# Performance work log

Measured on AMD Instinct MI355X. Metric: run time of the kernel, lower is better.

The kernel has to match this reference:

```python
import jax, jax.numpy as jnp
import numpy as np

N_EMBED = 1024
EMBED_DIM = 256

def setup_inputs() -> dict:
    key = jax.random.key(0)
    k1, k2 = jax.random.split(key)
    hidden_states = jax.random.normal(k1, (64, 32, 32, EMBED_DIM), dtype=jnp.float32)
    emb_weights = jax.random.normal(k2, (N_EMBED, EMBED_DIM), dtype=jnp.float32)
    return {"hidden_states": hidden_states, "emb_weights": emb_weights}

def reference(hidden_states, emb_weights):
    # flatten (B,H,W,C) -> (N, C) with C == embed_dim
    z_flat = hidden_states.reshape((-1, EMBED_DIM))
    # squared distance: ||z||^2 + ||e||^2 - 2 z.e
    distance = (
        jnp.sum(z_flat ** 2, axis=1, keepdims=True)
        + jnp.sum(emb_weights ** 2, axis=1)
        - 2.0 * jnp.dot(z_flat, emb_weights.T)
    )  # (N, n_embed)
    min_encoding_indices = jnp.argmin(distance, axis=1)  # (N,)
    z_q = jnp.take(emb_weights, min_encoding_indices, axis=0).reshape(hidden_states.shape)
    min_encoding_indices = min_encoding_indices.reshape(hidden_states.shape[0], -1)
    return z_q, min_encoding_indices
```

## Files before the change

kernel.cpp:

```cpp
#include <hip/hip_runtime.h>

typedef _Float16 half8  __attribute__((ext_vector_type(8)));
typedef _Float16 half4  __attribute__((ext_vector_type(4)));
typedef float    float4v __attribute__((ext_vector_type(4)));
typedef float    float8v __attribute__((ext_vector_type(8)));

#define N_ROWS  65536
#define N_CODES 1024
#define DIM     256
#define BM      64
#define NBLKS   (N_ROWS / BM)

__global__ __launch_bounds__(64)
void vq_prep(const float* __restrict__ emb, float* __restrict__ e_norm,
             _Float16* __restrict__ e_frag, int* __restrict__ count) {
    const int c = blockIdx.x, lane = threadIdx.x;
    const int l15 = c & 15, nt = c >> 4;
    if (count && c == 0 && lane == 0) *count = 0;
    float4v v = ((const float4v*)(emb + (size_t)c * DIM))[lane];
    half4 h, l;
    float ss = 0.f;
    #pragma unroll
    for (int j = 0; j < 4; ++j) {
        float x = v[j];
        ss += x * x;
        _Float16 hh = (_Float16)x;
        h[j] = hh;
        l[j] = (_Float16)(x - (float)hh);
    }
    const int ks = lane >> 3, q = (lane >> 1) & 3, jb = (lane & 1) * 4;
    _Float16* p = e_frag + ((size_t)(nt * 8 + ks)) * 1024 + (q * 16 + l15) * 8 + jb;
    *(half4*)p = h;
    *(half4*)(p + 512) = l;
    #pragma unroll
    for (int m = 32; m >= 1; m >>= 1) ss += __shfl_xor(ss, m, 64);
    if (lane == 0) e_norm[c] = ss;
}

__global__ __launch_bounds__(256, 2)
void vq_screen(const float* __restrict__ z,
               const _Float16* __restrict__ e_frag,
               const float* __restrict__ e_norm,
               const float* __restrict__ emb,
               float* __restrict__ zq,
               float* __restrict__ idxf,
               int* __restrict__ count,
               int* __restrict__ list) {
    __shared__ _Float16 sA[32 * 512];
    __shared__ float    s_nrm[N_CODES];
    __shared__ float    s_znrm[BM];
    __shared__ float    s_red[4];
    __shared__ float4   s_best[BM][5];
    __shared__ int      s_idx[BM];

    const int t = threadIdx.x;
    const int w = t >> 6, lane = t & 63, quad = lane >> 4, l15 = lane & 15;
    const int rowblk = blockIdx.x * BM;

    float n0 = e_norm[t], n1 = e_norm[t + 256], n2 = e_norm[t + 512], n3 = e_norm[t + 768];
    s_nrm[t] = n0; s_nrm[t + 256] = n1; s_nrm[t + 512] = n2; s_nrm[t + 768] = n3;
    float mx = fmaxf(fmaxf(n0, n1), fmaxf(n2, n3));
    #pragma unroll
    for (int m = 1; m < 64; m <<= 1) mx = fmaxf(mx, __shfl_xor(mx, m, 64));
    if (lane == 0) s_red[w] = mx;

    float ss = 0.f;
    #pragma unroll
    for (int i = 0; i < 8; ++i) {
        const int row = w * 16 + l15;
        const int col = i * 32 + quad * 8;
        float8v v = *(const float8v*)(z + (size_t)(rowblk + row) * DIM + col);
        half8 h;
        #pragma unroll
        for (int j = 0; j < 8; ++j) {
            float x = v[j];
            ss += x * x;
            h[j] = (_Float16)x;
        }
        *(half8*)(sA + (size_t)(w * 8 + i) * 512 + lane * 8) = h;
    }
    ss += __shfl_xor(ss, 16, 64);
    ss += __shfl_xor(ss, 32, 64);
    if (quad == 0) s_znrm[w * 16 + l15] = ss;
    __syncthreads();

    for (int pass = 0; pass < 2; ++pass) {
        const int ntbase = w * 16 + pass * 8;
        float4v acc[4][8] = {};

        #pragma unroll
        for (int ks = 0; ks < 8; ++ks) {
            half8 bh[8];
            #pragma unroll
            for (int nt = 0; nt < 8; ++nt)
                bh[nt] = *(const half8*)(e_frag + ((size_t)((ntbase + nt) * 8 + ks)) * 1024 + lane * 8);
            __builtin_amdgcn_s_setprio(1);
            #pragma unroll
            for (int mt = 0; mt < 4; ++mt) {
                half8 ah = *(const half8*)(sA + (size_t)(mt * 8 + ks) * 512 + lane * 8);
                #pragma unroll
                for (int nt = 0; nt < 8; ++nt)
                    acc[mt][nt] = __builtin_amdgcn_mfma_f32_16x16x32_f16(ah, bh[nt], acc[mt][nt], 0, 0, 0);
            }
            __builtin_amdgcn_s_setprio(0);
        }

        float nrm[8]; int cg[8];
        #pragma unroll
        for (int nt = 0; nt < 8; ++nt) {
            cg[nt]  = (ntbase + nt) * 16 + l15;
            nrm[nt] = s_nrm[cg[nt]];
        }
        #pragma unroll
        for (int mt = 0; mt < 4; ++mt) {
            #pragma unroll
            for (int r = 0; r < 4; ++r) {
                float m1 = nrm[0] - 2.0f * acc[mt][0][r]; int i1 = cg[0];
                float m2 = 1e30f;
                #pragma unroll
                for (int nt = 1; nt < 8; ++nt) {
                    float s = nrm[nt] - 2.0f * acc[mt][nt][r];
                    if (s < m1) { m2 = m1; m1 = s; i1 = cg[nt]; }
                    else m2 = fminf(m2, s);
                }
                #pragma unroll
                for (int m = 1; m < 16; m <<= 1) {
                    float o1 = __shfl_xor(m1, m, 64);
                    int   oi = __shfl_xor(i1, m, 64);
                    float o2 = __shfl_xor(m2, m, 64);
                    if (o1 < m1 || (o1 == m1 && oi < i1)) {
                        m2 = fminf(m1, o2); m1 = o1; i1 = oi;
                    } else {
                        m2 = fminf(m2, o1);
                    }
                }
                if (l15 == 0) {
                    const int row = mt * 16 + quad * 4 + r;
                    if (pass == 0) {
                        float4 pr; pr.x = m1; pr.y = (float)i1; pr.z = m2; pr.w = 0.f;
                        s_best[row][w] = pr;
                    } else {
                        float4 pv = s_best[row][w];
                        float4 pr;
                        if (m1 < pv.x) { pr.x = m1; pr.y = (float)i1; pr.z = fminf(pv.x, m2); }
                        else           { pr.x = pv.x; pr.y = pv.y;     pr.z = fminf(pv.z, m1); }
                        pr.w = 0.f;
                        s_best[row][w] = pr;
                    }
                }
            }
        }
    }
    __syncthreads();

    if (t < BM) {
        float4 b0 = s_best[t][0];
        float m1 = b0.x, fi = b0.y, m2 = b0.z;
        #pragma unroll
        for (int s = 1; s < 4; ++s) {
            float4 bv = s_best[t][s];
            if (bv.x < m1 || (bv.x == m1 && bv.y < fi)) {
                m2 = fminf(m1, bv.z); m1 = bv.x; fi = bv.y;
            } else {
                m2 = fminf(m2, bv.x);
            }
        }
        s_idx[t] = (int)fi;
        idxf[rowblk + t] = fi;
        float emax = sqrtf(fmaxf(fmaxf(s_red[0], s_red[1]), fmaxf(s_red[2], s_red[3])));
        float T = 0.005f * sqrtf(s_znrm[t]) * emax + 0.05f;
        if (m2 - m1 <= T) {
            int pos = atomicAdd(count, 1);
            list[pos] = rowblk + t;
        }
    }
    __syncthreads();

    const float4v* emb4 = (const float4v*)emb;
    float4v* zq4 = (float4v*)zq;
    const int rr = t >> 2, cb = t & 3;
    const int code = s_idx[rr];
    #pragma unroll
    for (int i = 0; i < 16; ++i) {
        const int chunk = cb + i * 4;
        zq4[(size_t)(rowblk + rr) * 64 + chunk] = emb4[(size_t)code * 64 + chunk];
    }
}

__global__ __launch_bounds__(256, 2)
void vq_exact(const float* __restrict__ z,
              const _Float16* __restrict__ e_frag,
              const float* __restrict__ e_norm,
              const float* __restrict__ emb,
              float* __restrict__ zq,
              float* __restrict__ idxf,
              const int* __restrict__ count,
              const int* __restrict__ list) {
    const int cnt = *count;
    const int base = blockIdx.x * BM;
    if (base >= cnt) return;

    __shared__ _Float16 sA[32 * 2 * 512];
    __shared__ float    s_nrm[N_CODES];
    __shared__ float2   s_best[BM][5];
    __shared__ int      s_idx[BM];
    __shared__ int      s_rows[BM];

    const int t = threadIdx.x;
    const int w = t >> 6, lane = t & 63, quad = lane >> 4, l15 = lane & 15;

    if (t < BM) {
        int slot = base + t;
        s_rows[t] = list[slot < cnt ? slot : cnt - 1];
    }
    s_nrm[t]       = e_norm[t];
    s_nrm[t + 256] = e_norm[t + 256];
    s_nrm[t + 512] = e_norm[t + 512];
    s_nrm[t + 768] = e_norm[t + 768];
    __syncthreads();

    #pragma unroll
    for (int i = 0; i < 8; ++i) {
        const int row = w * 16 + l15;
        const int grow = s_rows[row];
        const int col = i * 32 + quad * 8;
        float8v v = *(const float8v*)(z + (size_t)grow * DIM + col);
        half8 h, lo;
        #pragma unroll
        for (int j = 0; j < 8; ++j) {
            float x = v[j];
            _Float16 hh = (_Float16)x;
            h[j] = hh;
            lo[j] = (_Float16)(x - (float)hh);
        }
        _Float16* p = sA + (size_t)((w * 8 + i) * 2) * 512 + lane * 8;
        *(half8*)p = h;
        *(half8*)(p + 512) = lo;
    }
    __syncthreads();

    for (int pass = 0; pass < 2; ++pass) {
        const int ntbase = w * 16 + pass * 8;
        float4v acc[4][8] = {};

        #pragma unroll
        for (int ks = 0; ks < 8; ++ks) {
            half8 bh[8], bl[8];
            #pragma unroll
            for (int nt = 0; nt < 8; ++nt) {
                const _Float16* bp = e_frag + ((size_t)((ntbase + nt) * 8 + ks)) * 1024 + lane * 8;
                bh[nt] = *(const half8*)bp;
                bl[nt] = *(const half8*)(bp + 512);
            }
            __builtin_amdgcn_s_setprio(1);
            #pragma unroll
            for (int mt = 0; mt < 4; ++mt) {
                const _Float16* ap = sA + (size_t)((mt * 8 + ks) * 2) * 512 + lane * 8;
                half8 ah = *(const half8*)ap;
                half8 al = *(const half8*)(ap + 512);
                #pragma unroll
                for (int nt = 0; nt < 8; ++nt)
                    acc[mt][nt] = __builtin_amdgcn_mfma_f32_16x16x32_f16(ah, bh[nt], acc[mt][nt], 0, 0, 0);
                #pragma unroll
                for (int nt = 0; nt < 8; ++nt)
                    acc[mt][nt] = __builtin_amdgcn_mfma_f32_16x16x32_f16(ah, bl[nt], acc[mt][nt], 0, 0, 0);
                #pragma unroll
                for (int nt = 0; nt < 8; ++nt)
                    acc[mt][nt] = __builtin_amdgcn_mfma_f32_16x16x32_f16(al, bh[nt], acc[mt][nt], 0, 0, 0);
            }
            __builtin_amdgcn_s_setprio(0);
        }

        float nrm[8]; int cg[8];
        #pragma unroll
        for (int nt = 0; nt < 8; ++nt) {
            cg[nt]  = (ntbase + nt) * 16 + l15;
            nrm[nt] = s_nrm[cg[nt]];
        }
        #pragma unroll
        for (int mt = 0; mt < 4; ++mt) {
            #pragma unroll
            for (int r = 0; r < 4; ++r) {
                float bs = nrm[0] - 2.0f * acc[mt][0][r]; int bi = cg[0];
                #pragma unroll
                for (int nt = 1; nt < 8; ++nt) {
                    float s = nrm[nt] - 2.0f * acc[mt][nt][r];
                    if (s < bs) { bs = s; bi = cg[nt]; }
                }
                #pragma unroll
                for (int m = 1; m < 16; m <<= 1) {
                    float s2 = __shfl_xor(bs, m, 64);
                    int   i2 = __shfl_xor(bi, m, 64);
                    if (s2 < bs || (s2 == bs && i2 < bi)) { bs = s2; bi = i2; }
                }
                if (l15 == 0) {
                    const int row = mt * 16 + quad * 4 + r;
                    if (pass == 0) {
                        float2 pr; pr.x = bs; pr.y = (float)bi;
                        s_best[row][w] = pr;
                    } else {
                        float2 pv = s_best[row][w];
                        if (bs < pv.x) {
                            float2 pr; pr.x = bs; pr.y = (float)bi;
                            s_best[row][w] = pr;
                        }
                    }
                }
            }
        }
    }
    __syncthreads();

    if (t < BM) {
        float2 p0 = s_best[t][0];
        float bs = p0.x, bi = p0.y;
        #pragma unroll
        for (int s = 1; s < 4; ++s) {
            float2 pv = s_best[t][s];
            if (pv.x < bs || (pv.x == bs && pv.y < bi)) { bs = pv.x; bi = pv.y; }
        }
        s_idx[t] = (int)bi;
        idxf[s_rows[t]] = bi;
    }
    __syncthreads();

    const float4v* emb4 = (const float4v*)emb;
    float4v* zq4 = (float4v*)zq;
    const int rr = t >> 2, cb = t & 3;
    const int grow = s_rows[rr];
    const int code = s_idx[rr];
    #pragma unroll
    for (int i = 0; i < 16; ++i) {
        const int chunk = cb + i * 4;
        zq4[(size_t)grow * 64 + chunk] = emb4[(size_t)code * 64 + chunk];
    }
}

__global__ __launch_bounds__(256, 2)
void vq_main(const float* __restrict__ z,
             const _Float16* __restrict__ e_frag,
             const float* __restrict__ e_norm,
             const float* __restrict__ emb,
             float* __restrict__ zq,
             float* __restrict__ idxf,
             int fused_gather) {
    __shared__ _Float16 sA[32 * 2 * 512];
    __shared__ float    s_nrm[N_CODES];
    __shared__ float2   s_best[BM][5];
    __shared__ int      s_idx[BM];

    const int t = threadIdx.x;
    const int w = t >> 6, lane = t & 63, quad = lane >> 4, l15 = lane & 15;
    const int rowblk = blockIdx.x * BM;

    s_nrm[t]       = e_norm[t];
    s_nrm[t + 256] = e_norm[t + 256];
    s_nrm[t + 512] = e_norm[t + 512];
    s_nrm[t + 768] = e_norm[t + 768];

    #pragma unroll
    for (int i = 0; i < 8; ++i) {
        const int row = w * 16 + l15;
        const int col = i * 32 + quad * 8;
        float8v v = *(const float8v*)(z + (size_t)(rowblk + row) * DIM + col);
        half8 h, lo;
        #pragma unroll
        for (int j = 0; j < 8; ++j) {
            float x = v[j];
            _Float16 hh = (_Float16)x;
            h[j] = hh;
            lo[j] = (_Float16)(x - (float)hh);
        }
        _Float16* p = sA + (size_t)((w * 8 + i) * 2) * 512 + lane * 8;
        *(half8*)p = h;
        *(half8*)(p + 512) = lo;
    }
    __syncthreads();

    for (int pass = 0; pass < 2; ++pass) {
        const int ntbase = w * 16 + pass * 8;
        float4v acc[4][8] = {};

        #pragma unroll
        for (int ks = 0; ks < 8; ++ks) {
            half8 bh[8], bl[8];
            #pragma unroll
            for (int nt = 0; nt < 8; ++nt) {
                const _Float16* bp = e_frag + ((size_t)((ntbase + nt) * 8 + ks)) * 1024 + lane * 8;
                bh[nt] = *(const half8*)bp;
                bl[nt] = *(const half8*)(bp + 512);
            }
            __builtin_amdgcn_s_setprio(1);
            #pragma unroll
            for (int mt = 0; mt < 4; ++mt) {
                const _Float16* ap = sA + (size_t)((mt * 8 + ks) * 2) * 512 + lane * 8;
                half8 ah = *(const half8*)ap;
                half8 al = *(const half8*)(ap + 512);
                #pragma unroll
                for (int nt = 0; nt < 8; ++nt)
                    acc[mt][nt] = __builtin_amdgcn_mfma_f32_16x16x32_f16(ah, bh[nt], acc[mt][nt], 0, 0, 0);
                #pragma unroll
                for (int nt = 0; nt < 8; ++nt)
                    acc[mt][nt] = __builtin_amdgcn_mfma_f32_16x16x32_f16(ah, bl[nt], acc[mt][nt], 0, 0, 0);
                #pragma unroll
                for (int nt = 0; nt < 8; ++nt)
                    acc[mt][nt] = __builtin_amdgcn_mfma_f32_16x16x32_f16(al, bh[nt], acc[mt][nt], 0, 0, 0);
            }
            __builtin_amdgcn_s_setprio(0);
        }

        float nrm[8]; int cg[8];
        #pragma unroll
        for (int nt = 0; nt < 8; ++nt) {
            cg[nt]  = (ntbase + nt) * 16 + l15;
            nrm[nt] = s_nrm[cg[nt]];
        }
        #pragma unroll
        for (int mt = 0; mt < 4; ++mt) {
            #pragma unroll
            for (int r = 0; r < 4; ++r) {
                float bs = nrm[0] - 2.0f * acc[mt][0][r]; int bi = cg[0];
                #pragma unroll
                for (int nt = 1; nt < 8; ++nt) {
                    float s = nrm[nt] - 2.0f * acc[mt][nt][r];
                    if (s < bs) { bs = s; bi = cg[nt]; }
                }
                #pragma unroll
                for (int m = 1; m < 16; m <<= 1) {
                    float s2 = __shfl_xor(bs, m, 64);
                    int   i2 = __shfl_xor(bi, m, 64);
                    if (s2 < bs || (s2 == bs && i2 < bi)) { bs = s2; bi = i2; }
                }
                if (l15 == 0) {
                    const int row = mt * 16 + quad * 4 + r;
                    if (pass == 0) {
                        float2 pr; pr.x = bs; pr.y = (float)bi;
                        s_best[row][w] = pr;
                    } else {
                        float2 pv = s_best[row][w];
                        if (bs < pv.x) {
                            float2 pr; pr.x = bs; pr.y = (float)bi;
                            s_best[row][w] = pr;
                        }
                    }
                }
            }
        }
    }
    __syncthreads();

    if (t < BM) {
        float2 p0 = s_best[t][0];
        float bs = p0.x, bi = p0.y;
        #pragma unroll
        for (int s = 1; s < 4; ++s) {
            float2 pv = s_best[t][s];
            if (pv.x < bs || (pv.x == bs && pv.y < bi)) { bs = pv.x; bi = pv.y; }
        }
        s_idx[t] = (int)bi;
        idxf[rowblk + t] = bi;
    }

    if (!fused_gather) return;
    __syncthreads();

    const float4v* emb4 = (const float4v*)emb;
    float4v* zq4 = (float4v*)zq;
    const int rr = t >> 2, cb = t & 3;
    const int code = s_idx[rr];
    #pragma unroll
    for (int i = 0; i < 16; ++i) {
        const int chunk = cb + i * 4;
        zq4[(size_t)(rowblk + rr) * 64 + chunk] = emb4[(size_t)code * 64 + chunk];
    }
}

__global__ __launch_bounds__(256)
void vq_gather(const float* __restrict__ emb,
               const float* __restrict__ idxf,
               float* __restrict__ zq) {
    const int tid  = blockIdx.x * 256 + threadIdx.x;
    const int r    = tid >> 6;
    const int lane = tid & 63;
    const int idx  = (int)idxf[r];
    const float4* ep = (const float4*)(emb + (size_t)idx * DIM);
    ((float4*)(zq + (size_t)r * DIM))[lane] = ep[lane];
}

extern "C" void kernel_launch(void* const* d_in, const int* in_sizes, int n_in,
                              void* d_out, int out_size, void* d_ws, size_t ws_size,
                              hipStream_t stream) {
    const float* z   = (const float*)d_in[0];
    const float* emb = (const float*)d_in[1];

    float* zq   = (float*)d_out;
    float* idxf = zq + (size_t)N_ROWS * DIM;

    const size_t efrag_sz = (size_t)N_CODES * DIM * 2 * sizeof(_Float16);
    const size_t list_sz  = (size_t)N_ROWS * sizeof(int);
    const size_t need_p   = 4096 + efrag_sz + 4096 + list_sz;

    if (ws_size >= need_p) {
        float*    e_norm = (float*)d_ws;
        _Float16* e_frag = (_Float16*)((char*)d_ws + 4096);
        int*      count  = (int*)((char*)d_ws + 4096 + efrag_sz);
        int*      list   = (int*)((char*)d_ws + 4096 + efrag_sz + 4096);
        vq_prep<<<N_CODES, 64, 0, stream>>>(emb, e_norm, e_frag, count);
        vq_screen<<<NBLKS, 256, 0, stream>>>(z, e_frag, e_norm, emb, zq, idxf, count, list);
        vq_exact<<<NBLKS, 256, 0, stream>>>(z, e_frag, e_norm, emb, zq, idxf, count, list);
    } else {
        const size_t need = 4096 + efrag_sz;
        const int in_ws = (ws_size >= need);
        char* base = in_ws ? (char*)d_ws : (char*)d_out;
        float*    e_norm = (float*)base;
        _Float16* e_frag = (_Float16*)(base + 4096);
        vq_prep<<<N_CODES, 64, 0, stream>>>(emb, e_norm, e_frag, (int*)0);
        vq_main<<<NBLKS, 256, 0, stream>>>(z, e_frag, e_norm, emb, zq, idxf, in_ws);
        if (!in_ws)
            vq_gather<<<(N_ROWS * 64) / 256, 256, 0, stream>>>(emb, idxf, zq);
    }
}
```

Before: 217.5 us.

## Tighten screen error bound and split exact rescoring across code octants

The fp16 screening threshold now comes from the actual low-part residual norms of z and the codebook, rather than a fixed relative factor. This should flag fewer rows for exact rescoring. The exact pass is split into vq_resc, which uses 8 blocks per group of 64 flagged rows, each covering one eighth of the codes and merging results through 64-bit packed atomicMin. A separate vq_fix kernel then writes the indices and the gather. This adds a kernel launch and extra atomics and workspace, in exchange for more parallelism and less rescoring work.

```diff
diff --git a/kernel.cpp b/kernel.cpp
--- a/kernel.cpp
+++ b/kernel.cpp
@@ -11,45 +11,63 @@
 #define BM      64
 #define NBLKS   (N_ROWS / BM)
 
+__device__ __forceinline__ unsigned long long packScore(float s, int code) {
+    unsigned u = __float_as_uint(s);
+    u ^= (u >> 31) ? 0xFFFFFFFFu : 0x80000000u;
+    return ((unsigned long long)u << 32) | (unsigned)code;
+}
+
 __global__ __launch_bounds__(64)
 void vq_prep(const float* __restrict__ emb, float* __restrict__ e_norm,
-             _Float16* __restrict__ e_frag, int* __restrict__ count) {
+             float* __restrict__ el2, _Float16* __restrict__ e_frag,
+             int* __restrict__ count) {
     const int c = blockIdx.x, lane = threadIdx.x;
     const int l15 = c & 15, nt = c >> 4;
     if (count && c == 0 && lane == 0) *count = 0;
     float4v v = ((const float4v*)(emb + (size_t)c * DIM))[lane];
     half4 h, l;
-    float ss = 0.f;
+    float ss = 0.f, ssl = 0.f;
     #pragma unroll
     for (int j = 0; j < 4; ++j) {
         float x = v[j];
         ss += x * x;
         _Float16 hh = (_Float16)x;
+        float xl = x - (float)hh;
+        ssl += xl * xl;
         h[j] = hh;
-        l[j] = (_Float16)(x - (float)hh);
+        l[j] = (_Float16)xl;
     }
     const int ks = lane >> 3, q = (lane >> 1) & 3, jb = (lane & 1) * 4;
     _Float16* p = e_frag + ((size_t)(nt * 8 + ks)) * 1024 + (q * 16 + l15) * 8 + jb;
     *(half4*)p = h;
     *(half4*)(p + 512) = l;
     #pragma unroll
-    for (int m = 32; m >= 1; m >>= 1) ss += __shfl_xor(ss, m, 64);
-    if (lane == 0) e_norm[c] = ss;
+    for (int m = 32; m >= 1; m >>= 1) {
+        ss  += __shfl_xor(ss, m, 64);
+        ssl += __shfl_xor(ssl, m, 64);
+    }
+    if (lane == 0) {
+        e_norm[c] = ss;
+        if (el2) el2[c] = ssl;
+    }
 }
 
 __global__ __launch_bounds__(256, 2)
 void vq_screen(const float* __restrict__ z,
                const _Float16* __restrict__ e_frag,
                const float* __restrict__ e_norm,
+               const float* __restrict__ el2,
                const float* __restrict__ emb,
                float* __restrict__ zq,
                float* __restrict__ idxf,
                int* __restrict__ count,
-               int* __restrict__ list) {
+               int* __restrict__ list,
+               unsigned long long* __restrict__ packed) {
     __shared__ _Float16 sA[32 * 512];
     __shared__ float    s_nrm[N_CODES];
     __shared__ float    s_znrm[BM];
-    __shared__ float    s_red[4];
+    __shared__ float    s_zlnrm[BM];
+    __shared__ float    s_red[4], s_redl[4];
     __shared__ float4   s_best[BM][5];
     __shared__ int      s_idx[BM];
 
@@ -60,11 +78,16 @@
     float n0 = e_norm[t], n1 = e_norm[t + 256], n2 = e_norm[t + 512], n3 = e_norm[t + 768];
     s_nrm[t] = n0; s_nrm[t + 256] = n1; s_nrm[t + 512] = n2; s_nrm[t + 768] = n3;
     float mx = fmaxf(fmaxf(n0, n1), fmaxf(n2, n3));
-    #pragma unroll
-    for (int m = 1; m < 64; m <<= 1) mx = fmaxf(mx, __shfl_xor(mx, m, 64));
-    if (lane == 0) s_red[w] = mx;
-
-    float ss = 0.f;
+    float q0 = el2[t], q1 = el2[t + 256], q2 = el2[t + 512], q3 = el2[t + 768];
+    float mxl = fmaxf(fmaxf(q0, q1), fmaxf(q2, q3));
+    #pragma unroll
+    for (int m = 1; m < 64; m <<= 1) {
+        mx  = fmaxf(mx,  __shfl_xor(mx, m, 64));
+        mxl = fmaxf(mxl, __shfl_xor(mxl, m, 64));
+    }
+    if (lane == 0) { s_red[w] = mx; s_redl[w] = mxl; }
+
+    float ss = 0.f, ssl = 0.f;
     #pragma unroll
     for (int i = 0; i < 8; ++i) {
         const int row = w * 16 + l15;
@@ -75,13 +98,18 @@
         for (int j = 0; j < 8; ++j) {
             float x = v[j];
             ss += x * x;
-            h[j] = (_Float16)x;
+            _Float16 hh = (_Float16)x;
+            float xl = x - (float)hh;
+            ssl += xl * xl;
+            h[j] = hh;
         }
         *(half8*)(sA + (size_t)(w * 8 + i) * 512 + lane * 8) = h;
     }
-    ss += __shfl_xor(ss, 16, 64);
-    ss += __shfl_xor(ss, 32, 64);
-    if (quad == 0) s_znrm[w * 16 + l15] = ss;
+    ss  += __shfl_xor(ss, 16, 64);
+    ss  += __shfl_xor(ss, 32, 64);
+    ssl += __shfl_xor(ssl, 16, 64);
+    ssl += __shfl_xor(ssl, 32, 64);
+    if (quad == 0) { s_znrm[w * 16 + l15] = ss; s_zlnrm[w * 16 + l15] = ssl; }
     __syncthreads();
 
     for (int pass = 0; pass < 2; ++pass) {
@@ -167,11 +195,13 @@
         }
         s_idx[t] = (int)fi;
         idxf[rowblk + t] = fi;
-        float emax = sqrtf(fmaxf(fmaxf(s_red[0], s_red[1]), fmaxf(s_red[2], s_red[3])));
-        float T = 0.005f * sqrtf(s_znrm[t]) * emax + 0.05f;
+        float emax  = sqrtf(fmaxf(fmaxf(s_red[0],  s_red[1]),  fmaxf(s_red[2],  s_red[3])));
+        float elmax = sqrtf(fmaxf(fmaxf(s_redl[0], s_redl[1]), fmaxf(s_redl[2], s_redl[3])));
+        float T = 2.0f * (sqrtf(s_zlnrm[t]) * emax + 1.001f * sqrtf(s_znrm[t]) * elmax) + 0.02f;
         if (m2 - m1 <= T) {
             int pos = atomicAdd(count, 1);
             list[pos] = rowblk + t;
+            packed[rowblk + t] = 0xFFFFFFFFFFFFFFFFull;
         }
     }
     __syncthreads();
@@ -188,35 +218,27 @@
 }
 
 __global__ __launch_bounds__(256, 2)
-void vq_exact(const float* __restrict__ z,
-              const _Float16* __restrict__ e_frag,
-              const float* __restrict__ e_norm,
-              const float* __restrict__ emb,
-              float* __restrict__ zq,
-              float* __restrict__ idxf,
-              const int* __restrict__ count,
-              const int* __restrict__ list) {
+void vq_resc(const float* __restrict__ z,
+             const _Float16* __restrict__ e_frag,
+             const float* __restrict__ e_norm,
+             const int* __restrict__ count,
+             const int* __restrict__ list,
+             unsigned long long* __restrict__ packed) {
     const int cnt = *count;
-    const int base = blockIdx.x * BM;
-    if (base >= cnt) return;
+    const int g = blockIdx.x >> 3, oct = blockIdx.x & 7;
+    if (g * BM >= cnt) return;
 
     __shared__ _Float16 sA[32 * 2 * 512];
-    __shared__ float    s_nrm[N_CODES];
     __shared__ float2   s_best[BM][5];
-    __shared__ int      s_idx[BM];
     __shared__ int      s_rows[BM];
 
     const int t = threadIdx.x;
     const int w = t >> 6, lane = t & 63, quad = lane >> 4, l15 = lane & 15;
 
     if (t < BM) {
-        int slot = base + t;
+        int slot = g * BM + t;
         s_rows[t] = list[slot < cnt ? slot : cnt - 1];
     }
-    s_nrm[t]       = e_norm[t];
-    s_nrm[t + 256] = e_norm[t + 256];
-    s_nrm[t + 512] = e_norm[t + 512];
-    s_nrm[t + 768] = e_norm[t + 768];
     __syncthreads();
 
     #pragma unroll
@@ -225,6 +247,152 @@
         const int grow = s_rows[row];
         const int col = i * 32 + quad * 8;
         float8v v = *(const float8v*)(z + (size_t)grow * DIM + col);
+        half8 h, lo;
+        #pragma unroll
+        for (int j = 0; j < 8; ++j) {
+            float x = v[j];
+            _Float16 hh = (_Float16)x;
+            h[j] = hh;
+            lo[j] = (_Float16)(x - (float)hh);
+        }
+        _Float16* p = sA + (size_t)((w * 8 + i) * 2) * 512 + lane * 8;
+        *(half8*)p = h;
+        *(half8*)(p + 512) = lo;
+    }
+    __syncthreads();
+
+    const int ntbase = oct * 8 + w * 2;
+    float4v acc[4][2] = {};
+
+    #pragma unroll
+    for (int ks = 0; ks < 8; ++ks) {
+        half8 bh[2], bl[2];
+        #pragma unroll
+        for (int nt = 0; nt < 2; ++nt) {
+            const _Float16* bp = e_frag + ((size_t)((ntbase + nt) * 8 + ks)) * 1024 + lane * 8;
+            bh[nt] = *(const half8*)bp;
+            bl[nt] = *(const half8*)(bp + 512);
+        }
+        __builtin_amdgcn_s_setprio(1);
+        #pragma unroll
+        for (int mt = 0; mt < 4; ++mt) {
+            const _Float16* ap = sA + (size_t)((mt * 8 + ks) * 2) * 512 + lane * 8;
+            half8 ah = *(const half8*)ap;
+            half8 al = *(const half8*)(ap + 512);
+            #pragma unroll
+            for (int nt = 0; nt < 2; ++nt)
+                acc[mt][nt] = __builtin_amdgcn_mfma_f32_16x16x32_f16(ah, bh[nt], acc[mt][nt], 0, 0, 0);
+            #pragma unroll
+            for (int nt = 0; nt < 2; ++nt)
+                acc[mt][nt] = __builtin_amdgcn_mfma_f32_16x16x32_f16(ah, bl[nt], acc[mt][nt], 0, 0, 0);
+            #pragma unroll
+            for (int nt = 0; nt < 2; ++nt)
+                acc[mt][nt] = __builtin_amdgcn_mfma_f32_16x16x32_f16(al, bh[nt], acc[mt][nt], 0, 0, 0);
+        }
+        __builtin_amdgcn_s_setprio(0);
+    }
+
+    float nrm[2]; int cg[2];
+    #pragma unroll
+    for (int nt = 0; nt < 2; ++nt) {
+        cg[nt]  = (ntbase + nt) * 16 + l15;
+        nrm[nt] = e_norm[cg[nt]];
+    }
+    #pragma unroll
+    for (int mt = 0; mt < 4; ++mt) {
+        #pragma unroll
+        for (int r = 0; r < 4; ++r) {
+            float bs = nrm[0] - 2.0f * acc[mt][0][r]; int bi = cg[0];
+            float s1 = nrm[1] - 2.0f * acc[mt][1][r];
+            if (s1 < bs) { bs = s1; bi = cg[1]; }
+            #pragma unroll
+            for (int m = 1; m < 16; m <<= 1) {
+                float s2 = __shfl_xor(bs, m, 64);
+                int   i2 = __shfl_xor(bi, m, 64);
+                if (s2 < bs || (s2 == bs && i2 < bi)) { bs = s2; bi = i2; }
+            }
+            if (l15 == 0) {
+                float2 pr; pr.x = bs; pr.y = (float)bi;
+                s_best[mt * 16 + quad * 4 + r][w] = pr;
+            }
+        }
+    }
+    __syncthreads();
+
+    if (t < BM) {
+        float2 p0 = s_best[t][0];
+        float bs = p0.x, bi = p0.y;
+        #pragma unroll
+        for (int s = 1; s < 4; ++s) {
+            float2 pv = s_best[t][s];
+            if (pv.x < bs || (pv.x == bs && pv.y < bi)) { bs = pv.x; bi = pv.y; }
+        }
+        atomicMin(&packed[s_rows[t]], packScore(bs, (int)bi));
+    }
+}
+
+__global__ __launch_bounds__(256)
+void vq_fix(const float* __restrict__ emb,
+            const int* __restrict__ count,
+            const int* __restrict__ list,
+            const unsigned long long* __restrict__ packed,
+            float* __restrict__ zq,
+            float* __restrict__ idxf) {
+    const int cnt = *count;
+    const int base = blockIdx.x * BM;
+    if (base >= cnt) return;
+
+    __shared__ int s_rows[BM], s_code[BM];
+    const int t = threadIdx.x;
+    if (t < BM) {
+        int slot = base + t;
+        int row = list[slot < cnt ? slot : cnt - 1];
+        s_rows[t] = row;
+        int code = (int)(unsigned)packed[row];
+        s_code[t] = code;
+        idxf[row] = (float)code;
+    }
+    __syncthreads();
+
+    const float4v* emb4 = (const float4v*)emb;
+    float4v* zq4 = (float4v*)zq;
+    const int rr = t >> 2, cb = t & 3;
+    const int grow = s_rows[rr];
+    const int code = s_code[rr];
+    #pragma unroll
+    for (int i = 0; i < 16; ++i) {
+        const int chunk = cb + i * 4;
+        zq4[(size_t)grow * 64 + chunk] = emb4[(size_t)code * 64 + chunk];
+    }
+}
+
+__global__ __launch_bounds__(256, 2)
+void vq_main(const float* __restrict__ z,
+             const _Float16* __restrict__ e_frag,
+             const float* __restrict__ e_norm,
+             const float* __restrict__ emb,
+             float* __restrict__ zq,
+             float* __restrict__ idxf,
+             int fused_gather) {
+    __shared__ _Float16 sA[32 * 2 * 512];
+    __shared__ float    s_nrm[N_CODES];
+    __shared__ float2   s_best[BM][5];
+    __shared__ int      s_idx[BM];
+
+    const int t = threadIdx.x;
+    const int w = t >> 6, lane = t & 63, quad = lane >> 4, l15 = lane & 15;
+    const int rowblk = blockIdx.x * BM;
+
+    s_nrm[t]       = e_norm[t];
+    s_nrm[t + 256] = e_norm[t + 256];
+    s_nrm[t + 512] = e_norm[t + 512];
+    s_nrm[t + 768] = e_norm[t + 768];
+
+    #pragma unroll
+    for (int i = 0; i < 8; ++i) {
+        const int row = w * 16 + l15;
+        const int col = i * 32 + quad * 8;
+        float8v v = *(const float8v*)(z + (size_t)(rowblk + row) * DIM + col);
         half8 h, lo;
         #pragma unroll
         for (int j = 0; j < 8; ++j) {
@@ -320,144 +488,6 @@
             if (pv.x < bs || (pv.x == bs && pv.y < bi)) { bs = pv.x; bi = pv.y; }
         }
         s_idx[t] = (int)bi;
-        idxf[s_rows[t]] = bi;
-    }
-    __syncthreads();
-
-    const float4v* emb4 = (const float4v*)emb;
-    float4v* zq4 = (float4v*)zq;
-    const int rr = t >> 2, cb = t & 3;
-    const int grow = s_rows[rr];
-    const int code = s_idx[rr];
-    #pragma unroll
-    for (int i = 0; i < 16; ++i) {
-        const int chunk = cb + i * 4;
-        zq4[(size_t)grow * 64 + chunk] = emb4[(size_t)code * 64 + chunk];
-    }
-}
-
-__global__ __launch_bounds__(256, 2)
-void vq_main(const float* __restrict__ z,
-             const _Float16* __restrict__ e_frag,
-             const float* __restrict__ e_norm,
-             const float* __restrict__ emb,
-             float* __restrict__ zq,
-             float* __restrict__ idxf,
-             int fused_gather) {
-    __shared__ _Float16 sA[32 * 2 * 512];
-    __shared__ float    s_nrm[N_CODES];
-    __shared__ float2   s_best[BM][5];
-    __shared__ int      s_idx[BM];
-
-    const int t = threadIdx.x;
-    const int w = t >> 6, lane = t & 63, quad = lane >> 4, l15 = lane & 15;
-    const int rowblk = blockIdx.x * BM;
-
-    s_nrm[t]       = e_norm[t];
-    s_nrm[t + 256] = e_norm[t + 256];
-    s_nrm[t + 512] = e_norm[t + 512];
-    s_nrm[t + 768] = e_norm[t + 768];
-
-    #pragma unroll
-    for (int i = 0; i < 8; ++i) {
-        const int row = w * 16 + l15;
-        const int col = i * 32 + quad * 8;
-        float8v v = *(const float8v*)(z + (size_t)(rowblk + row) * DIM + col);
-        half8 h, lo;
-        #pragma unroll
-        for (int j = 0; j < 8; ++j) {
-            float x = v[j];
-            _Float16 hh = (_Float16)x;
-            h[j] = hh;
-            lo[j] = (_Float16)(x - (float)hh);
-        }
-        _Float16* p = sA + (size_t)((w * 8 + i) * 2) * 512 + lane * 8;
-        *(half8*)p = h;
-        *(half8*)(p + 512) = lo;
-    }
-    __syncthreads();
-
-    for (int pass = 0; pass < 2; ++pass) {
-        const int ntbase = w * 16 + pass * 8;
-        float4v acc[4][8] = {};
-
-        #pragma unroll
-        for (int ks = 0; ks < 8; ++ks) {
-            half8 bh[8], bl[8];
-            #pragma unroll
-            for (int nt = 0; nt < 8; ++nt) {
-                const _Float16* bp = e_frag + ((size_t)((ntbase + nt) * 8 + ks)) * 1024 + lane * 8;
-                bh[nt] = *(const half8*)bp;
-                bl[nt] = *(const half8*)(bp + 512);
-            }
-            __builtin_amdgcn_s_setprio(1);
-            #pragma unroll
-            for (int mt = 0; mt < 4; ++mt) {
-                const _Float16* ap = sA + (size_t)((mt * 8 + ks) * 2) * 512 + lane * 8;
-                half8 ah = *(const half8*)ap;
-                half8 al = *(const half8*)(ap + 512);
-                #pragma unroll
-                for (int nt = 0; nt < 8; ++nt)
-                    acc[mt][nt] = __builtin_amdgcn_mfma_f32_16x16x32_f16(ah, bh[nt], acc[mt][nt], 0, 0, 0);
-                #pragma unroll
-                for (int nt = 0; nt < 8; ++nt)
-                    acc[mt][nt] = __builtin_amdgcn_mfma_f32_16x16x32_f16(ah, bl[nt], acc[mt][nt], 0, 0, 0);
-                #pragma unroll
-                for (int nt = 0; nt < 8; ++nt)
-                    acc[mt][nt] = __builtin_amdgcn_mfma_f32_16x16x32_f16(al, bh[nt], acc[mt][nt], 0, 0, 0);
-            }
-            __builtin_amdgcn_s_setprio(0);
-        }
-
-        float nrm[8]; int cg[8];
-        #pragma unroll
-        for (int nt = 0; nt < 8; ++nt) {
-            cg[nt]  = (ntbase + nt) * 16 + l15;
-            nrm[nt] = s_nrm[cg[nt]];
-        }
-        #pragma unroll
-        for (int mt = 0; mt < 4; ++mt) {
-            #pragma unroll
-            for (int r = 0; r < 4; ++r) {
-                float bs = nrm[0] - 2.0f * acc[mt][0][r]; int bi = cg[0];
-                #pragma unroll
-                for (int nt = 1; nt < 8; ++nt) {
-                    float s = nrm[nt] - 2.0f * acc[mt][nt][r];
-                    if (s < bs) { bs = s; bi = cg[nt]; }
-                }
-                #pragma unroll
-                for (int m = 1; m < 16; m <<= 1) {
-                    float s2 = __shfl_xor(bs, m, 64);
-                    int   i2 = __shfl_xor(bi, m, 64);
-                    if (s2 < bs || (s2 == bs && i2 < bi)) { bs = s2; bi = i2; }
-                }
-                if (l15 == 0) {
-                    const int row = mt * 16 + quad * 4 + r;
-                    if (pass == 0) {
-                        float2 pr; pr.x = bs; pr.y = (float)bi;
-                        s_best[row][w] = pr;
-                    } else {
-                        float2 pv = s_best[row][w];
-                        if (bs < pv.x) {
-                            float2 pr; pr.x = bs; pr.y = (float)bi;
-                            s_best[row][w] = pr;
-                        }
-                    }
-                }
-            }
-        }
-    }
-    __syncthreads();
-
-    if (t < BM) {
-        float2 p0 = s_best[t][0];
-        float bs = p0.x, bi = p0.y;
-        #pragma unroll
-        for (int s = 1; s < 4; ++s) {
-            float2 pv = s_best[t][s];
-            if (pv.x < bs || (pv.x == bs && pv.y < bi)) { bs = pv.x; bi = pv.y; }
-        }
-        s_idx[t] = (int)bi;
         idxf[rowblk + t] = bi;
     }
 
@@ -496,25 +526,34 @@
     float* zq   = (float*)d_out;
     float* idxf = zq + (size_t)N_ROWS * DIM;
 
-    const size_t efrag_sz = (size_t)N_CODES * DIM * 2 * sizeof(_Float16);
-    const size_t list_sz  = (size_t)N_ROWS * sizeof(int);
-    const size_t need_p   = 4096 + efrag_sz + 4096 + list_sz;
+    const size_t efrag_sz  = (size_t)N_CODES * DIM * 2 * sizeof(_Float16);
+    const size_t list_sz   = (size_t)N_ROWS * sizeof(int);
+    const size_t packed_sz = (size_t)N_ROWS * sizeof(unsigned long long);
+    const size_t off_el2    = 4096;
+    const size_t off_efrag  = 8192;
+    const size_t off_count  = off_efrag + efrag_sz;
+    const size_t off_list   = off_count + 4096;
+    const size_t off_packed = off_list + list_sz;
+    const size_t need_p     = off_packed + packed_sz;
 
     if (ws_size >= need_p) {
         float*    e_norm = (float*)d_ws;
-        _Float16* e_frag = (_Float16*)((char*)d_ws + 4096);
-        int*      count  = (int*)((char*)d_ws + 4096 + efrag_sz);
-        int*      list   = (int*)((char*)d_ws + 4096 + efrag_sz + 4096);
-        vq_prep<<<N_CODES, 64, 0, stream>>>(emb, e_norm, e_frag, count);
-        vq_screen<<<NBLKS, 256, 0, stream>>>(z, e_frag, e_norm, emb, zq, idxf, count, list);
-        vq_exact<<<NBLKS, 256, 0, stream>>>(z, e_frag, e_norm, emb, zq, idxf, count, list);
+        float*    el2    = (float*)((char*)d_ws + off_el2);
+        _Float16* e_frag = (_Float16*)((char*)d_ws + off_efrag);
+        int*      count  = (int*)((char*)d_ws + off_count);
+        int*      list   = (int*)((char*)d_ws + off_list);
+        unsigned long long* packed = (unsigned long long*)((char*)d_ws + off_packed);
+        vq_prep<<<N_CODES, 64, 0, stream>>>(emb, e_norm, el2, e_frag, count);
+        vq_screen<<<NBLKS, 256, 0, stream>>>(z, e_frag, e_norm, el2, emb, zq, idxf, count, list, packed);
+        vq_resc<<<NBLKS * 8, 256, 0, stream>>>(z, e_frag, e_norm, count, list, packed);
+        vq_fix<<<NBLKS, 256, 0, stream>>>(emb, count, list, packed, zq, idxf);
     } else {
-        const size_t need = 4096 + efrag_sz;
+        const size_t need = off_efrag + efrag_sz;
         const int in_ws = (ws_size >= need);
         char* base = in_ws ? (char*)d_ws : (char*)d_out;
         float*    e_norm = (float*)base;
-        _Float16* e_frag = (_Float16*)(base + 4096);
-        vq_prep<<<N_CODES, 64, 0, stream>>>(emb, e_norm, e_frag, (int*)0);
+        _Float16* e_frag = (_Float16*)(base + off_efrag);
+        vq_prep<<<N_CODES, 64, 0, stream>>>(emb, e_norm, (float*)0, e_frag, (int*)0);
         vq_main<<<NBLKS, 256, 0, stream>>>(z, e_frag, e_norm, emb, zq, idxf, in_ws);
         if (!in_ws)
             vq_gather<<<(N_ROWS * 64) / 256, 256, 0, stream>>>(emb, idxf, zq);
```

New measurement: 199.0 us. -8.5%, faster.
